# Kernel tuning notes

Measured on AMD Instinct MI355X. Metric: run time of the kernel, lower is better.

## Reference

```python
import jax, jax.numpy as jnp
import numpy as np

RES = 128
SIGMA = 2
EPS = 1e-6
# 8 corner combinations of a voxel, [8, 3], static numpy constant
COMBOS = np.stack(np.meshgrid(*[[0, 1]] * 3, indexing='ij'), axis=-1).reshape(8, 3)


def _corner_idx_weights(points, res):
    """Trilinear corner indices and weights.
    points: [B, N, 3] in [0,1). Returns idx [B,N,8,3] int32, w [B,N,8].
    Matches torch code: weight for a corner = prod over dims of distance to
    the OPPOSITE corner coordinate, divided by voxel size.
    """
    pr = points * res
    lo = jnp.floor(pr)
    li = lo.astype(jnp.int32) % res           # lower index (mod res)
    ui = jnp.ceil(pr).astype(jnp.int32) % res  # upper index (mod res)
    frac = pr - lo                             # fractional offset in voxel
    c = COMBOS[None, None]                     # [1,1,8,3]
    idx = jnp.where(c == 1, ui[:, :, None, :], li[:, :, None, :])   # [B,N,8,3]
    wd = jnp.where(c == 1, frac[:, :, None, :], 1.0 - frac[:, :, None, :])
    w = jnp.prod(wd, axis=-1)                  # [B,N,8]
    return idx, w


def point_rasterization(points, features, res):
    """Scatter-add trilinear splatting. Returns [B, F, res, res, res]."""
    B, N, _ = points.shape
    F = features.shape[2]
    idx, w = _corner_idx_weights(points, res)
    vals = w[..., None] * features[:, :, None, :]          # [B,N,8,F]
    flat = (idx[..., 0] * res + idx[..., 1]) * res + idx[..., 2]  # [B,N,8]

    def scat(fl, v):  # fl [N,8], v [N,8,F]
        g = jnp.zeros((res * res * res, F), dtype=v.dtype)
        g = g.at[fl.reshape(-1)].add(v.reshape(-1, F))
        return g.T.reshape(F, res, res, res)

    return jax.vmap(scat)(flat, vals)


def grid_interpolation(field, points, res):
    """Trilinear gather. field: [B, res, res, res], points: [B,N,3] -> [B,N]."""
    idx, w = _corner_idx_weights(points, res)

    def gath(f, ix):  # f [res,res,res], ix [N,8,3]
        return f[ix[..., 0], ix[..., 1], ix[..., 2]]  # [N,8]

    vals = jax.vmap(gath)(field, idx)  # [B,N,8]
    return jnp.sum(w * vals, axis=-1)  # [B,N]


def _fft_freq_grid(res):
    f = jnp.fft.fftfreq(res, d=1.0 / res).astype(jnp.float32)  # integer frequencies
    return jnp.stack(jnp.meshgrid(f, f, f, indexing='ij'), axis=-1)  # [res,res,res,3]


def setup_inputs() -> dict:
    key = jax.random.key(0)
    k1, k2 = jax.random.split(key)
    points = jax.random.uniform(k1, (1, 250000, 3), dtype=jnp.float32) * 0.999
    normals = jax.random.normal(k2, (1, 250000, 3), dtype=jnp.float32)
    return {"points": points, "normals": normals}


def reference(points, normals):
    res = RES
    u = _fft_freq_grid(res)                                  # [X,Y,Z,3]
    u_sq = jnp.sum(u ** 2, axis=-1)                          # [X,Y,Z]
    g = jnp.exp(-2.0 * (SIGMA / res) ** 2 * u_sq)            # gaussian smoothing

    v = point_rasterization(points, normals, res)            # [B,3,X,Y,Z]
    v_tilde = jnp.fft.fftn(v, axes=(2, 3, 4)).transpose(0, 2, 3, 4, 1)  # [B,X,Y,Z,3]

    vec = jnp.sum(u[None] * v_tilde, axis=-1) / (u_sq[None] + EPS)      # [B,X,Y,Z]
    chi_tilde = g[None] * ((-1j / (2 * jnp.pi)) * vec)
    chi_prime = jnp.fft.ifftn(chi_tilde, axes=(1, 2, 3)).real            # [B,X,Y,Z]

    chi_c = grid_interpolation(chi_prime, points, res)        # [B,N]
    vecf = chi_prime - jnp.mean(chi_c, axis=-1)[:, None, None, None]
    chi_0 = vecf[:, 0, 0, 0]                                  # [B]
    chi = (0.5 / jnp.abs(chi_0))[:, None, None, None] * vecf
    return chi
```

## Files before the change

kernel.cpp:

```cpp
#include <hip/hip_runtime.h>
#include <math.h>

#define RES 128
#define RES2 (RES*RES)
#define RES3 (RES*RES*RES)
#define NROWS 16384

__device__ __forceinline__ int brev7(unsigned x){ return (int)(__brev(x) >> 25); }
__device__ __forceinline__ float freq_of(int s){ int k = brev7((unsigned)s); return (float)(k < 64 ? k : k - 128); }
__device__ __forceinline__ float2 cmul(float2 a, float2 b){
    return make_float2(a.x*b.x - a.y*b.y, a.x*b.y + a.y*b.x);
}
__device__ __forceinline__ float2 twd(float ang){ float s, c; __sincosf(ang, &s, &c); return make_float2(c, s); }

struct TW { float2 s64; float2 w[6]; };
__device__ __forceinline__ TW make_tw(int tt){
    TW t;
    t.s64 = twd(-(float)M_PI * (float)tt * (1.f/64.f));
    #pragma unroll
    for (int i = 0; i < 6; i++){
        int h = 32 >> i;
        t.w[i] = twd(-(float)M_PI * (float)(tt & (h - 1)) / (float)h);
    }
    return t;
}

__device__ __forceinline__ void dif128_t(float2& r0, float2& r1, int tt, const TW& tw){
    {
        float2 a = r0, b = r1;
        r0 = make_float2(a.x + b.x, a.y + b.y);
        float2 d = make_float2(a.x - b.x, a.y - b.y);
        r1 = cmul(d, tw.s64);
    }
    #pragma unroll
    for (int i = 0; i < 6; i++){
        int h = 32 >> i;
        int bit = tt & h;
        float2 w = tw.w[i];
        float2 o0 = make_float2(__shfl_xor(r0.x, h), __shfl_xor(r0.y, h));
        float2 o1 = make_float2(__shfl_xor(r1.x, h), __shfl_xor(r1.y, h));
        if (!bit){
            r0.x += o0.x; r0.y += o0.y;
            r1.x += o1.x; r1.y += o1.y;
        } else {
            r0 = cmul(make_float2(o0.x - r0.x, o0.y - r0.y), w);
            r1 = cmul(make_float2(o1.x - r1.x, o1.y - r1.y), w);
        }
    }
}

__device__ __forceinline__ void dit128_t(float2& r0, float2& r1, int tt, const TW& tw){
    #pragma unroll
    for (int i = 5; i >= 0; i--){
        int h = 32 >> i;
        int bit = tt & h;
        float2 w = make_float2(tw.w[i].x, -tw.w[i].y);
        float2 o0 = make_float2(__shfl_xor(r0.x, h), __shfl_xor(r0.y, h));
        float2 o1 = make_float2(__shfl_xor(r1.x, h), __shfl_xor(r1.y, h));
        if (!bit){
            float2 t0 = cmul(o0, w), t1 = cmul(o1, w);
            r0.x += t0.x; r0.y += t0.y;
            r1.x += t1.x; r1.y += t1.y;
        } else {
            float2 t0 = cmul(r0, w), t1 = cmul(r1, w);
            r0 = make_float2(o0.x - t0.x, o0.y - t0.y);
            r1 = make_float2(o1.x - t1.x, o1.y - t1.y);
        }
    }
    {
        float2 w = make_float2(tw.s64.x, -tw.s64.y);
        float2 b = cmul(r1, w);
        float2 a = r0;
        r0 = make_float2(a.x + b.x, a.y + b.y);
        r1 = make_float2(a.x - b.x, a.y - b.y);
    }
}

__global__ void hist_kernel(const float* __restrict__ pts, int* __restrict__ counts, int N){
    int i = blockIdx.x * blockDim.x + threadIdx.x;
    if (i >= N) return;
    float prx = pts[3*i] * RES, pry = pts[3*i+1] * RES;
    int lx = ((int)floorf(prx)) & 127, ly = ((int)floorf(pry)) & 127;
    atomicAdd(&counts[(lx << 7) | ly], 1);
}

__global__ __launch_bounds__(1024) void rowscan(const int* __restrict__ counts,
                                                int* __restrict__ starts,
                                                int* __restrict__ cursors){
    __shared__ int buf[2][1024];
    int t = threadIdx.x;
    int c[16];
    int base = t * 16;
    int s = 0;
    #pragma unroll
    for (int k = 0; k < 16; k++){ c[k] = counts[base + k]; s += c[k]; }
    buf[0][t] = s;
    __syncthreads();
    int cur = 0;
    for (int d = 1; d < 1024; d <<= 1){
        int v = buf[cur][t];
        if (t >= d) v += buf[cur][t - d];
        buf[cur ^ 1][t] = v;
        cur ^= 1;
        __syncthreads();
    }
    int incl = buf[cur][t];
    int run = incl - s;
    #pragma unroll
    for (int k = 0; k < 16; k++){ starts[base + k] = run; cursors[base + k] = run; run += c[k]; }
    if (t == 1023) starts[NROWS] = incl;
}

__global__ void scatter_sorted(const float* __restrict__ pts, const float* __restrict__ nrm,
                               int* __restrict__ cursors, float* __restrict__ sorted, int N){
    int i = blockIdx.x * blockDim.x + threadIdx.x;
    if (i >= N) return;
    float px = pts[3*i], py = pts[3*i+1], pz = pts[3*i+2];
    int lx = ((int)floorf(px * RES)) & 127, ly = ((int)floorf(py * RES)) & 127;
    int pos = atomicAdd(&cursors[(lx << 7) | ly], 1);
    float* q = sorted + (size_t)pos * 6;
    q[0] = px; q[1] = py; q[2] = pz;
    q[3] = nrm[3*i]; q[4] = nrm[3*i+1]; q[5] = nrm[3*i+2];
}

__global__ __launch_bounds__(768) void gather_z(const float* __restrict__ sorted,
                                                const int* __restrict__ starts,
                                                float2* __restrict__ zF){
    __shared__ float col[3][4][RES];
    int x  = blockIdx.x >> 5;
    int y0 = (blockIdx.x & 31) << 2;
    int t = threadIdx.x;
    ((float*)col)[t] = 0.f;
    ((float*)col)[t + 768] = 0.f;
    __syncthreads();
    int xm = (x + 127) & 127;
    int ybase = (y0 == 0) ? 127 : (y0 - 1);
    int n1 = (y0 == 0) ? 1 : 5;
    int n2 = 5 - n1;
    int a_s[4], a_e[4];
    { int r = (xm << 7) | ybase; a_s[0] = starts[r]; a_e[0] = starts[r + n1]; }
    { int r = (xm << 7);         a_s[1] = starts[r]; a_e[1] = starts[r + n2]; }
    { int r = (x  << 7) | ybase; a_s[2] = starts[r]; a_e[2] = starts[r + n1]; }
    { int r = (x  << 7);         a_s[3] = starts[r]; a_e[3] = starts[r + n2]; }
    int p1 = a_e[0] - a_s[0];
    int p2 = p1 + (a_e[1] - a_s[1]);
    int p3 = p2 + (a_e[2] - a_s[2]);
    int tot = p3 + (a_e[3] - a_s[3]);
    for (int base = 0; base < tot; base += 768){
        int k = base + t;
        if (k < tot){
            int i;
            if      (k < p1) i = a_s[0] + k;
            else if (k < p2) i = a_s[1] + (k - p1);
            else if (k < p3) i = a_s[2] + (k - p2);
            else             i = a_s[3] + (k - p3);
            const float* q = sorted + (size_t)i * 6;
            float prx = q[0]*RES, pry = q[1]*RES, prz = q[2]*RES;
            float flx = floorf(prx), fly = floorf(pry), flz = floorf(prz);
            float fx = prx - flx, fy = pry - fly, fz = prz - flz;
            int lxp = ((int)flx) & 127, lyp = ((int)fly) & 127, lz = ((int)flz) & 127;
            float wx = (lxp == x) ? (1.f - fx) : fx;
            int z1 = (lz + 1) & 127;
            float n0 = q[3], nv1 = q[4], nv2 = q[5];
            int jA = (lyp - y0) & 127;
            int jB = (jA + 1) & 127;
            if (jA < 4){
                float wy = wx * (1.f - fy);
                float w0 = wy * (1.f - fz), w1 = wy * fz;
                atomicAdd(&col[0][jA][lz], w0*n0);  atomicAdd(&col[0][jA][z1], w1*n0);
                atomicAdd(&col[1][jA][lz], w0*nv1); atomicAdd(&col[1][jA][z1], w1*nv1);
                atomicAdd(&col[2][jA][lz], w0*nv2); atomicAdd(&col[2][jA][z1], w1*nv2);
            }
            if (jB < 4){
                float wy = wx * fy;
                float w0 = wy * (1.f - fz), w1 = wy * fz;
                atomicAdd(&col[0][jB][lz], w0*n0);  atomicAdd(&col[0][jB][z1], w1*n0);
                atomicAdd(&col[1][jB][lz], w0*nv1); atomicAdd(&col[1][jB][z1], w1*nv1);
                atomicAdd(&col[2][jB][lz], w0*nv2); atomicAdd(&col[2][jB][z1], w1*nv2);
            }
        }
    }
    __syncthreads();
    int w = t >> 6, tt = t & 63;
    int c = w >> 2, j = w & 3;
    TW tw = make_tw(tt);
    float2 r0 = make_float2(col[c][j][tt], 0.f);
    float2 r1 = make_float2(col[c][j][tt + 64], 0.f);
    dif128_t(r0, r1, tt, tw);
    float2* qo = zF + (size_t)c * RES3 + (((size_t)x << 14) | ((size_t)(y0 + j) << 7));
    qo[tt] = r0; qo[tt + 64] = r1;
}

__global__ __launch_bounds__(1024) void mega_y(const float2* __restrict__ zF,
                                               float2* __restrict__ bufA,
                                               float2* __restrict__ bufB){
    __shared__ float2 tile[16][130];
    int t = threadIdx.x;
    int x = blockIdx.x >> 3, z0 = (blockIdx.x & 7) << 4;
    size_t base = ((size_t)x << 14) + (size_t)z0;
    int y0 = t >> 4, zz = t & 15, y1 = y0 + 64;
    size_t i0 = base + ((size_t)y0 << 7) + zz;
    size_t i1 = base + ((size_t)y1 << 7) + zz;
    int w = t >> 6, tt = t & 63;
    TW tw = make_tw(tt);
    tile[zz][y0] = zF[RES3 + i0]; tile[zz][y1] = zF[RES3 + i1];
    __syncthreads();
    float2 A0 = tile[w][tt], A1 = tile[w][tt + 64];
    __syncthreads();
    dif128_t(A0, A1, tt, tw);
    { float f0 = freq_of(tt), f1 = freq_of(tt + 64);
      A0.x *= f0; A0.y *= f0; A1.x *= f1; A1.y *= f1; }
    tile[zz][y0] = zF[2*(size_t)RES3 + i0]; tile[zz][y1] = zF[2*(size_t)RES3 + i1];
    __syncthreads();
    float2 C0 = tile[w][tt], C1 = tile[w][tt + 64];
    __syncthreads();
    dif128_t(C0, C1, tt, tw);
    { float fz = freq_of(z0 + w);
      A0.x += fz*C0.x; A0.y += fz*C0.y; A1.x += fz*C1.x; A1.y += fz*C1.y; }
    tile[zz][y0] = zF[i0]; tile[zz][y1] = zF[i1];
    __syncthreads();
    float2 B0 = tile[w][tt], B1 = tile[w][tt + 64];
    __syncthreads();
    dif128_t(B0, B1, tt, tw);
    tile[w][tt] = A0; tile[w][tt + 64] = A1;
    __syncthreads();
    bufA[i0] = tile[zz][y0]; bufA[i1] = tile[zz][y1];
    __syncthreads();
    tile[w][tt] = B0; tile[w][tt + 64] = B1;
    __syncthreads();
    bufB[i0] = tile[zz][y0]; bufB[i1] = tile[zz][y1];
}

__global__ __launch_bounds__(1024) void x_mega(const float2* __restrict__ bufB,
                                               float2* __restrict__ bufA){
    __shared__ float2 tA[16][130];
    __shared__ float2 tB[16][130];
    int t = threadIdx.x;
    int y = blockIdx.x >> 3, z0 = (blockIdx.x & 7) << 4;
    size_t base = ((size_t)y << 7) + (size_t)z0;
    int x0 = t >> 4, zz = t & 15;
    int x1 = x0 + 64;
    size_t g0 = base + ((size_t)x0 << 14) + zz;
    size_t g1 = base + ((size_t)x1 << 14) + zz;
    tA[zz][x0] = bufA[g0]; tA[zz][x1] = bufA[g1];
    tB[zz][x0] = bufB[g0]; tB[zz][x1] = bufB[g1];
    __syncthreads();
    int w = t >> 6, tt = t & 63;
    TW tw = make_tw(tt);
    float2 a0 = tA[w][tt], a1 = tA[w][tt + 64];
    float2 b0 = tB[w][tt], b1 = tB[w][tt + 64];
    dif128_t(a0, a1, tt, tw);
    dif128_t(b0, b1, tt, tw);
    float fy = freq_of(y), fz = freq_of(z0 + w);
    float fyz = fy*fy + fz*fz;
    const float K = -2.f * (2.f/128.f) * (2.f/128.f);
    {
        float fx = freq_of(tt);
        float vx = a0.x + fx*b0.x, vy = a0.y + fx*b0.y;
        float usq = fx*fx + fyz;
        float s = __expf(K*usq) / ((usq + 1e-6f) * (2.f*(float)M_PI));
        a0 = make_float2(s*vy, -s*vx);
    }
    {
        float fx = freq_of(tt + 64);
        float vx = a1.x + fx*b1.x, vy = a1.y + fx*b1.y;
        float usq = fx*fx + fyz;
        float s = __expf(K*usq) / ((usq + 1e-6f) * (2.f*(float)M_PI));
        a1 = make_float2(s*vy, -s*vx);
    }
    dit128_t(a0, a1, tt, tw);
    tA[w][tt] = a0; tA[w][tt + 64] = a1;
    __syncthreads();
    bufA[g0] = tA[zz][x0];
    bufA[g1] = tA[zz][x1];
}

__global__ __launch_bounds__(1024) void inv_y(float2* __restrict__ data){
    __shared__ float2 tile[16][130];
    int t = threadIdx.x;
    int x = blockIdx.x >> 3, z0 = (blockIdx.x & 7) << 4;
    size_t base = ((size_t)x << 14) + (size_t)z0;
    int y0 = t >> 4, zz = t & 15, y1 = y0 + 64;
    size_t i0 = base + ((size_t)y0 << 7) + zz;
    size_t i1 = base + ((size_t)y1 << 7) + zz;
    tile[zz][y0] = data[i0]; tile[zz][y1] = data[i1];
    __syncthreads();
    int w = t >> 6, tt = t & 63;
    TW tw = make_tw(tt);
    float2 r0 = tile[w][tt], r1 = tile[w][tt + 64];
    dit128_t(r0, r1, tt, tw);
    tile[w][tt] = r0; tile[w][tt + 64] = r1;
    __syncthreads();
    data[i0] = tile[zz][y0]; data[i1] = tile[zz][y1];
}

__global__ __launch_bounds__(256) void inv_z_c2r(const float2* __restrict__ in, float* __restrict__ out){
    int t = threadIdx.x; int wid = t >> 6, tt = t & 63;
    size_t line = (size_t)blockIdx.x * 4 + wid;
    const float2* p = in + line * RES;
    TW tw = make_tw(tt);
    float2 r0 = p[tt], r1 = p[tt + 64];
    dit128_t(r0, r1, tt, tw);
    const float sc = 1.f / (float)RES3;
    float* q = out + line * RES;
    q[tt] = r0.x * sc; q[tt + 64] = r1.x * sc;
}

__global__ void interp_sum(const float* __restrict__ chi, const float* __restrict__ pts,
                           float* __restrict__ sum, int N){
    int i = blockIdx.x * blockDim.x + threadIdx.x;
    float val = 0.f;
    if (i < N){
        float px = pts[3*i], py = pts[3*i+1], pz = pts[3*i+2];
        float prx = px * RES, pry = py * RES, prz = pz * RES;
        float lox = floorf(prx), loy = floorf(pry), loz = floorf(prz);
        int lix = ((int)lox) & 127, liy = ((int)loy) & 127, liz = ((int)loz) & 127;
        int uix = ((int)ceilf(prx)) & 127, uiy = ((int)ceilf(pry)) & 127, uiz = ((int)ceilf(prz)) & 127;
        float fx = prx - lox, fy = pry - loy, fz = prz - loz;
        #pragma unroll
        for (int cx = 0; cx < 2; cx++){
            int ix = cx ? uix : lix;
            float wx = cx ? fx : 1.f - fx;
            #pragma unroll
            for (int cy = 0; cy < 2; cy++){
                int iy = cy ? uiy : liy;
                float wxy = wx * (cy ? fy : 1.f - fy);
                #pragma unroll
                for (int cz = 0; cz < 2; cz++){
                    int iz = cz ? uiz : liz;
                    float w = wxy * (cz ? fz : 1.f - fz);
                    val += w * chi[(ix << 14) + (iy << 7) + iz];
                }
            }
        }
    }
    __shared__ float red[256];
    int tid = threadIdx.x;
    red[tid] = val;
    __syncthreads();
    #pragma unroll
    for (int s2 = 128; s2 > 0; s2 >>= 1){
        if (tid < s2) red[tid] += red[tid + s2];
        __syncthreads();
    }
    if (tid == 0) atomicAdd(sum, red[0]);
}

__global__ void final_scale(const float* __restrict__ chi, const float* __restrict__ sum,
                            float* __restrict__ out, float invN){
    int i = blockIdx.x * blockDim.x + threadIdx.x;
    if (i >= RES3) return;
    float mean = sum[0] * invN;
    float sc = 0.5f / fabsf(chi[0] - mean);
    out[i] = sc * (chi[i] - mean);
}

extern "C" void kernel_launch(void* const* d_in, const int* in_sizes, int n_in,
                              void* d_out, int out_size, void* d_ws, size_t ws_size,
                              hipStream_t stream) {
    const float* points  = (const float*)d_in[0];
    const float* normals = (const float*)d_in[1];
    float* out = (float*)d_out;
    char* ws = (char*)d_ws;

    size_t off = 0;
    float2* zF     = (float2*)(ws + off); off += (size_t)3*RES3*8;
    float2* bufA   = (float2*)(ws + off); off += (size_t)RES3*8;
    float2* bufB   = (float2*)(ws + off); off += (size_t)RES3*8;
    float*  chiP   = (float*) (ws + off); off += (size_t)RES3*4;
    float*  sumb   = (float*) (ws + off); off += 64;
    int*    counts = (int*)   (ws + off); off += (size_t)NROWS*4;
    int*    starts = (int*)   (ws + off); off += (size_t)(NROWS+1)*4;
    int*    cursors= (int*)   (ws + off); off += (size_t)NROWS*4;
    float*  sorted = (float*) (ws + off);

    int N = in_sizes[0] / 3;

    hipMemsetAsync(counts, 0, (size_t)NROWS*4, stream);
    hipMemsetAsync(sumb, 0, 16, stream);

    hist_kernel<<<(N + 255)/256, 256, 0, stream>>>(points, counts, N);
    rowscan<<<1, 1024, 0, stream>>>(counts, starts, cursors);
    scatter_sorted<<<(N + 255)/256, 256, 0, stream>>>(points, normals, cursors, sorted, N);
    gather_z<<<128*32, 768, 0, stream>>>(sorted, starts, zF);

    mega_y<<<1024, 1024, 0, stream>>>(zF, bufA, bufB);
    x_mega<<<1024, 1024, 0, stream>>>(bufB, bufA);
    inv_y<<<1024, 1024, 0, stream>>>(bufA);
    inv_z_c2r<<<RES2/4, 256, 0, stream>>>(bufA, chiP);

    interp_sum<<<(N + 255)/256, 256, 0, stream>>>(chiP, points, sumb, N);
    final_scale<<<RES3/256, 256, 0, stream>>>(chiP, sumb, out, 1.0f / (float)N);
}
```

Measured before the change: 237.0 us.

## Widen gather_z y-strips, pad sorted points to float4, vectorize FFT transposes

The gather kernel now covers 32 y-rows per block instead of 4. Neighbour-row points are therefore re-read far less often, at the cost of a 48KB shared accumulator and fewer blocks (512). Sorted point records are padded to two float4 slots so loads and stores are vectorized. The y/x/inverse-y FFT kernels now load and store global data as float4 pairs of complex values rather than single float2s, to improve coalescing.

Measured after the change: 232.0 us. 1.02x faster.

```diff
diff --git a/kernel.cpp b/kernel.cpp
--- a/kernel.cpp
+++ b/kernel.cpp
@@ -5,6 +5,7 @@
 #define RES2 (RES*RES)
 #define RES3 (RES*RES*RES)
 #define NROWS 16384
+#define STRIPW 32
 
 __device__ __forceinline__ int brev7(unsigned x){ return (int)(__brev(x) >> 25); }
 __device__ __forceinline__ float freq_of(int s){ int k = brev7((unsigned)s); return (float)(k < 64 ? k : k - 128); }
@@ -112,31 +113,30 @@
 }
 
 __global__ void scatter_sorted(const float* __restrict__ pts, const float* __restrict__ nrm,
-                               int* __restrict__ cursors, float* __restrict__ sorted, int N){
+                               int* __restrict__ cursors, float4* __restrict__ sorted4, int N){
     int i = blockIdx.x * blockDim.x + threadIdx.x;
     if (i >= N) return;
     float px = pts[3*i], py = pts[3*i+1], pz = pts[3*i+2];
     int lx = ((int)floorf(px * RES)) & 127, ly = ((int)floorf(py * RES)) & 127;
     int pos = atomicAdd(&cursors[(lx << 7) | ly], 1);
-    float* q = sorted + (size_t)pos * 6;
-    q[0] = px; q[1] = py; q[2] = pz;
-    q[3] = nrm[3*i]; q[4] = nrm[3*i+1]; q[5] = nrm[3*i+2];
-}
-
-__global__ __launch_bounds__(768) void gather_z(const float* __restrict__ sorted,
+    sorted4[2*pos]     = make_float4(px, py, pz, nrm[3*i]);
+    sorted4[2*pos + 1] = make_float4(nrm[3*i+1], nrm[3*i+2], 0.f, 0.f);
+}
+
+__global__ __launch_bounds__(768) void gather_z(const float4* __restrict__ sorted4,
                                                 const int* __restrict__ starts,
                                                 float2* __restrict__ zF){
-    __shared__ float col[3][4][RES];
-    int x  = blockIdx.x >> 5;
-    int y0 = (blockIdx.x & 31) << 2;
+    __shared__ float col[3][STRIPW][RES];
+    int x  = blockIdx.x >> 2;
+    int y0 = (blockIdx.x & 3) << 5;
     int t = threadIdx.x;
-    ((float*)col)[t] = 0.f;
-    ((float*)col)[t + 768] = 0.f;
+    #pragma unroll
+    for (int k = 0; k < 16; k++) ((float*)col)[t + 768*k] = 0.f;
     __syncthreads();
     int xm = (x + 127) & 127;
     int ybase = (y0 == 0) ? 127 : (y0 - 1);
-    int n1 = (y0 == 0) ? 1 : 5;
-    int n2 = 5 - n1;
+    int n1 = (y0 == 0) ? 1 : 33;
+    int n2 = 33 - n1;
     int a_s[4], a_e[4];
     { int r = (xm << 7) | ybase; a_s[0] = starts[r]; a_e[0] = starts[r + n1]; }
     { int r = (xm << 7);         a_s[1] = starts[r]; a_e[1] = starts[r + n2]; }
@@ -154,24 +154,25 @@
             else if (k < p2) i = a_s[1] + (k - p1);
             else if (k < p3) i = a_s[2] + (k - p2);
             else             i = a_s[3] + (k - p3);
-            const float* q = sorted + (size_t)i * 6;
-            float prx = q[0]*RES, pry = q[1]*RES, prz = q[2]*RES;
+            float4 qa = sorted4[2*i];
+            float4 qb = sorted4[2*i + 1];
+            float prx = qa.x*RES, pry = qa.y*RES, prz = qa.z*RES;
             float flx = floorf(prx), fly = floorf(pry), flz = floorf(prz);
             float fx = prx - flx, fy = pry - fly, fz = prz - flz;
             int lxp = ((int)flx) & 127, lyp = ((int)fly) & 127, lz = ((int)flz) & 127;
             float wx = (lxp == x) ? (1.f - fx) : fx;
             int z1 = (lz + 1) & 127;
-            float n0 = q[3], nv1 = q[4], nv2 = q[5];
+            float n0 = qa.w, nv1 = qb.x, nv2 = qb.y;
             int jA = (lyp - y0) & 127;
             int jB = (jA + 1) & 127;
-            if (jA < 4){
+            if (jA < STRIPW){
                 float wy = wx * (1.f - fy);
                 float w0 = wy * (1.f - fz), w1 = wy * fz;
                 atomicAdd(&col[0][jA][lz], w0*n0);  atomicAdd(&col[0][jA][z1], w1*n0);
                 atomicAdd(&col[1][jA][lz], w0*nv1); atomicAdd(&col[1][jA][z1], w1*nv1);
                 atomicAdd(&col[2][jA][lz], w0*nv2); atomicAdd(&col[2][jA][z1], w1*nv2);
             }
-            if (jB < 4){
+            if (jB < STRIPW){
                 float wy = wx * fy;
                 float w0 = wy * (1.f - fz), w1 = wy * fz;
                 atomicAdd(&col[0][jB][lz], w0*n0);  atomicAdd(&col[0][jB][z1], w1*n0);
@@ -182,13 +183,17 @@
     }
     __syncthreads();
     int w = t >> 6, tt = t & 63;
-    int c = w >> 2, j = w & 3;
     TW tw = make_tw(tt);
-    float2 r0 = make_float2(col[c][j][tt], 0.f);
-    float2 r1 = make_float2(col[c][j][tt + 64], 0.f);
-    dif128_t(r0, r1, tt, tw);
-    float2* qo = zF + (size_t)c * RES3 + (((size_t)x << 14) | ((size_t)(y0 + j) << 7));
-    qo[tt] = r0; qo[tt + 64] = r1;
+    #pragma unroll
+    for (int r = 0; r < 8; r++){
+        int idx = r * 12 + w;
+        int c = idx >> 5, j = idx & 31;
+        float2 r0 = make_float2(col[c][j][tt], 0.f);
+        float2 r1 = make_float2(col[c][j][tt + 64], 0.f);
+        dif128_t(r0, r1, tt, tw);
+        float2* qo = zF + (size_t)c * RES3 + (((size_t)x << 14) | ((size_t)(y0 + j) << 7));
+        qo[tt] = r0; qo[tt + 64] = r1;
+    }
 }
 
 __global__ __launch_bounds__(1024) void mega_y(const float2* __restrict__ zF,
@@ -198,37 +203,43 @@
     int t = threadIdx.x;
     int x = blockIdx.x >> 3, z0 = (blockIdx.x & 7) << 4;
     size_t base = ((size_t)x << 14) + (size_t)z0;
-    int y0 = t >> 4, zz = t & 15, y1 = y0 + 64;
-    size_t i0 = base + ((size_t)y0 << 7) + zz;
-    size_t i1 = base + ((size_t)y1 << 7) + zz;
+    int yv = t >> 3;
+    int z2 = (t & 7) << 1;
+    size_t gi = base + ((size_t)yv << 7) + z2;
+    const float4* zF4 = (const float4*)zF;
+    float4 L1 = zF4[((size_t)RES3 + gi) >> 1];
+    float4 L2 = zF4[(2*(size_t)RES3 + gi) >> 1];
+    float4 L0 = zF4[gi >> 1];
     int w = t >> 6, tt = t & 63;
     TW tw = make_tw(tt);
-    tile[zz][y0] = zF[RES3 + i0]; tile[zz][y1] = zF[RES3 + i1];
+    tile[z2][yv] = make_float2(L1.x, L1.y); tile[z2+1][yv] = make_float2(L1.z, L1.w);
     __syncthreads();
     float2 A0 = tile[w][tt], A1 = tile[w][tt + 64];
     __syncthreads();
     dif128_t(A0, A1, tt, tw);
     { float f0 = freq_of(tt), f1 = freq_of(tt + 64);
       A0.x *= f0; A0.y *= f0; A1.x *= f1; A1.y *= f1; }
-    tile[zz][y0] = zF[2*(size_t)RES3 + i0]; tile[zz][y1] = zF[2*(size_t)RES3 + i1];
+    tile[z2][yv] = make_float2(L2.x, L2.y); tile[z2+1][yv] = make_float2(L2.z, L2.w);
     __syncthreads();
     float2 C0 = tile[w][tt], C1 = tile[w][tt + 64];
     __syncthreads();
     dif128_t(C0, C1, tt, tw);
     { float fz = freq_of(z0 + w);
       A0.x += fz*C0.x; A0.y += fz*C0.y; A1.x += fz*C1.x; A1.y += fz*C1.y; }
-    tile[zz][y0] = zF[i0]; tile[zz][y1] = zF[i1];
+    tile[z2][yv] = make_float2(L0.x, L0.y); tile[z2+1][yv] = make_float2(L0.z, L0.w);
     __syncthreads();
     float2 B0 = tile[w][tt], B1 = tile[w][tt + 64];
     __syncthreads();
     dif128_t(B0, B1, tt, tw);
     tile[w][tt] = A0; tile[w][tt + 64] = A1;
     __syncthreads();
-    bufA[i0] = tile[zz][y0]; bufA[i1] = tile[zz][y1];
+    { float2 a = tile[z2][yv], b = tile[z2+1][yv];
+      ((float4*)bufA)[gi >> 1] = make_float4(a.x, a.y, b.x, b.y); }
     __syncthreads();
     tile[w][tt] = B0; tile[w][tt + 64] = B1;
     __syncthreads();
-    bufB[i0] = tile[zz][y0]; bufB[i1] = tile[zz][y1];
+    { float2 a = tile[z2][yv], b = tile[z2+1][yv];
+      ((float4*)bufB)[gi >> 1] = make_float4(a.x, a.y, b.x, b.y); }
 }
 
 __global__ __launch_bounds__(1024) void x_mega(const float2* __restrict__ bufB,
@@ -238,12 +249,12 @@
     int t = threadIdx.x;
     int y = blockIdx.x >> 3, z0 = (blockIdx.x & 7) << 4;
     size_t base = ((size_t)y << 7) + (size_t)z0;
-    int x0 = t >> 4, zz = t & 15;
-    int x1 = x0 + 64;
-    size_t g0 = base + ((size_t)x0 << 14) + zz;
-    size_t g1 = base + ((size_t)x1 << 14) + zz;
-    tA[zz][x0] = bufA[g0]; tA[zz][x1] = bufA[g1];
-    tB[zz][x0] = bufB[g0]; tB[zz][x1] = bufB[g1];
+    int xv = t >> 3, z2 = (t & 7) << 1;
+    size_t gi = base + ((size_t)xv << 14) + z2;
+    float4 LA = ((const float4*)bufA)[gi >> 1];
+    float4 LB = ((const float4*)bufB)[gi >> 1];
+    tA[z2][xv] = make_float2(LA.x, LA.y); tA[z2+1][xv] = make_float2(LA.z, LA.w);
+    tB[z2][xv] = make_float2(LB.x, LB.y); tB[z2+1][xv] = make_float2(LB.z, LB.w);
     __syncthreads();
     int w = t >> 6, tt = t & 63;
     TW tw = make_tw(tt);
@@ -271,8 +282,8 @@
     dit128_t(a0, a1, tt, tw);
     tA[w][tt] = a0; tA[w][tt + 64] = a1;
     __syncthreads();
-    bufA[g0] = tA[zz][x0];
-    bufA[g1] = tA[zz][x1];
+    { float2 a = tA[z2][xv], b = tA[z2+1][xv];
+      ((float4*)bufA)[gi >> 1] = make_float4(a.x, a.y, b.x, b.y); }
 }
 
 __global__ __launch_bounds__(1024) void inv_y(float2* __restrict__ data){
@@ -280,10 +291,10 @@
     int t = threadIdx.x;
     int x = blockIdx.x >> 3, z0 = (blockIdx.x & 7) << 4;
     size_t base = ((size_t)x << 14) + (size_t)z0;
-    int y0 = t >> 4, zz = t & 15, y1 = y0 + 64;
-    size_t i0 = base + ((size_t)y0 << 7) + zz;
-    size_t i1 = base + ((size_t)y1 << 7) + zz;
-    tile[zz][y0] = data[i0]; tile[zz][y1] = data[i1];
+    int yv = t >> 3, z2 = (t & 7) << 1;
+    size_t gi = base + ((size_t)yv << 7) + z2;
+    float4 L = ((const float4*)data)[gi >> 1];
+    tile[z2][yv] = make_float2(L.x, L.y); tile[z2+1][yv] = make_float2(L.z, L.w);
     __syncthreads();
     int w = t >> 6, tt = t & 63;
     TW tw = make_tw(tt);
@@ -291,7 +302,8 @@
     dit128_t(r0, r1, tt, tw);
     tile[w][tt] = r0; tile[w][tt + 64] = r1;
     __syncthreads();
-    data[i0] = tile[zz][y0]; data[i1] = tile[zz][y1];
+    { float2 a = tile[z2][yv], b = tile[z2+1][yv];
+      ((float4*)data)[gi >> 1] = make_float4(a.x, a.y, b.x, b.y); }
 }
 
 __global__ __launch_bounds__(256) void inv_z_c2r(const float2* __restrict__ in, float* __restrict__ out){
@@ -372,7 +384,8 @@
     int*    counts = (int*)   (ws + off); off += (size_t)NROWS*4;
     int*    starts = (int*)   (ws + off); off += (size_t)(NROWS+1)*4;
     int*    cursors= (int*)   (ws + off); off += (size_t)NROWS*4;
-    float*  sorted = (float*) (ws + off);
+    off = (off + 15) & ~(size_t)15;
+    float4* sorted4 = (float4*)(ws + off);
 
     int N = in_sizes[0] / 3;
 
@@ -381,8 +394,8 @@
 
     hist_kernel<<<(N + 255)/256, 256, 0, stream>>>(points, counts, N);
     rowscan<<<1, 1024, 0, stream>>>(counts, starts, cursors);
-    scatter_sorted<<<(N + 255)/256, 256, 0, stream>>>(points, normals, cursors, sorted, N);
-    gather_z<<<128*32, 768, 0, stream>>>(sorted, starts, zF);
+    scatter_sorted<<<(N + 255)/256, 256, 0, stream>>>(points, normals, cursors, sorted4, N);
+    gather_z<<<128*4, 768, 0, stream>>>(sorted4, starts, zF);
 
     mega_y<<<1024, 1024, 0, stream>>>(zF, bufA, bufB);
     x_mega<<<1024, 1024, 0, stream>>>(bufB, bufA);
```
